# Optimization experiments

Measured on AMD Instinct MI355X. Metric: run time of the kernel, lower is better.

Reference implementation:

```python
import jax, jax.numpy as jnp
import numpy as np

T, B, INPUT, HIDDEN, OUTPUT = 512, 128, 256, 512, 128

def setup_inputs() -> dict:
    key = jax.random.key(0)
    k1, k2, k3 = jax.random.split(key, 3)
    fan_in = INPUT + HIDDEN
    bound = 1.0 / np.sqrt(fan_in)
    x = jax.random.normal(k1, (T, B, INPUT), dtype=jnp.float32)
    W = jax.random.uniform(k2, (HIDDEN, fan_in), minval=-bound, maxval=bound, dtype=jnp.float32)
    b = jax.random.uniform(k3, (HIDDEN,), minval=-bound, maxval=bound, dtype=jnp.float32)
    return {"x": x, "W": W, "b": b}

def reference(x, W, b):
    # W: [H, INPUT+H] (torch Linear layout); split into input and hidden parts
    Wx = W[:, :INPUT]   # [H, I]
    Wh = W[:, INPUT:]   # [H, H]
    h0 = jnp.zeros((x.shape[1], Wh.shape[0]), dtype=x.dtype)
    # precompute input projections for all steps: [T, B, H]
    xp = jnp.einsum('tbi,hi->tbh', x, Wx) + b

    def step(h, xp_t):
        h_new = jnp.tanh(xp_t + h @ Wh.T)
        return h_new, h_new

    _, Hs = jax.lax.scan(step, h0, xp)
    return jnp.concatenate([h0[None], Hs], axis=0)  # [T+1, B, H]
```

## Files before the change

### kernel.cpp

```cpp
#include <hip/hip_runtime.h>
#include <hip/hip_bf16.h>
#include <hip/hip_fp16.h>
#include <stdint.h>

#define T_STEPS 512
#define BATCH   128
#define NIN     256
#define HID     512

typedef _Float16 f16x2 __attribute__((ext_vector_type(2)));
typedef unsigned int u32x4 __attribute__((ext_vector_type(4)));

__device__ __forceinline__ float fdot2u(uint32_t a, uint32_t b, float c) {
#if __has_builtin(__builtin_amdgcn_fdot2)
  return __builtin_amdgcn_fdot2(__builtin_bit_cast(f16x2, a),
                                __builtin_bit_cast(f16x2, b), c, false);
#else
  __half2 ha = __builtin_bit_cast(__half2, a);
  __half2 hb = __builtin_bit_cast(__half2, b);
  return c + __half2float(ha.x) * __half2float(hb.x)
           + __half2float(ha.y) * __half2float(hb.y);
#endif
}

__device__ __forceinline__ float dot8v(u32x4 w, u32x4 x, float a) {
  a = fdot2u(w.x, x.x, a);
  a = fdot2u(w.y, x.y, a);
  a = fdot2u(w.z, x.z, a);
  a = fdot2u(w.w, x.w, a);
  return a;
}

__device__ __forceinline__ float dot8(uint4 w, uint4 x, float a) {
  a = fdot2u(w.x, x.x, a);
  a = fdot2u(w.y, x.y, a);
  a = fdot2u(w.z, x.z, a);
  a = fdot2u(w.w, x.w, a);
  return a;
}

__global__ void prep_w(const float* __restrict__ W,
                       __half* __restrict__ Wx, __half* __restrict__ Wh) {
  int idx = blockIdx.x * 256 + threadIdx.x;
  int h = idx / (NIN + HID);
  int c = idx - h * (NIN + HID);
  float v = W[idx];
  if (c < NIN) Wx[h * NIN + c] = __float2half(v);
  else         Wh[h * HID + (c - NIN)] = __float2half(v);
}

__launch_bounds__(256)
__global__ void gemm_xp(const float* __restrict__ x,
                        const __half* __restrict__ Wx,
                        const float* __restrict__ bias,
                        float* __restrict__ xp) {
  __shared__ __align__(16) __half xs[32][256];

  const int bid = blockIdx.x;
  const int m0 = (bid >> 1) * 32;
  const int n0 = (bid & 1) * 256;
  const int tid = threadIdx.x;

  {
    int r = tid >> 3, cb = (tid & 7) * 32;
    const float* src = x + (size_t)(m0 + r) * NIN + cb;
    union { __half h[8]; uint4 u; } cv;
#pragma unroll
    for (int i = 0; i < 4; ++i) {
      float4 f0 = *(const float4*)(src + i * 8);
      float4 f1 = *(const float4*)(src + i * 8 + 4);
      cv.h[0] = __float2half(f0.x); cv.h[1] = __float2half(f0.y);
      cv.h[2] = __float2half(f0.z); cv.h[3] = __float2half(f0.w);
      cv.h[4] = __float2half(f1.x); cv.h[5] = __float2half(f1.y);
      cv.h[6] = __float2half(f1.z); cv.h[7] = __float2half(f1.w);
      *(uint4*)(void*)&xs[r][cb + i * 8] = cv.u;
    }
  }
  __syncthreads();

  const int rg = tid >> 6;
  const int c0 = tid & 63;

  float acc[8][4];
#pragma unroll
  for (int r = 0; r < 8; ++r)
#pragma unroll
    for (int j = 0; j < 4; ++j) acc[r][j] = 0.f;

  for (int kc = 0; kc < NIN; kc += 32) {
    uint4 w[4][4];
#pragma unroll
    for (int j = 0; j < 4; ++j) {
      const __half* wp = Wx + (size_t)(n0 + c0 + 64 * j) * NIN + kc;
#pragma unroll
      for (int i = 0; i < 4; ++i) w[j][i] = *(const uint4*)(wp + i * 8);
    }
#pragma unroll
    for (int r = 0; r < 8; ++r) {
      uint4 xv[4];
#pragma unroll
      for (int i = 0; i < 4; ++i)
        xv[i] = *(const uint4*)(const void*)&xs[rg * 8 + r][kc + i * 8];
#pragma unroll
      for (int j = 0; j < 4; ++j)
#pragma unroll
        for (int i = 0; i < 4; ++i) acc[r][j] = dot8(w[j][i], xv[i], acc[r][j]);
    }
  }

  float bj[4];
#pragma unroll
  for (int j = 0; j < 4; ++j) bj[j] = bias[n0 + c0 + 64 * j];
#pragma unroll
  for (int r = 0; r < 8; ++r) {
    float* dst = xp + (size_t)(m0 + rg * 8 + r) * HID + n0 + c0;
#pragma unroll
    for (int j = 0; j < 4; ++j) dst[64 * j] = acc[r][j] + bj[j];
  }
}

#define HCH 72
#define PST 520
__launch_bounds__(512, 2)
__global__ void rnn_scan(const __half* __restrict__ Wh, float* io) {
  __shared__ __align__(16) char  whl[131072];
  __shared__ __align__(16) float part[8 * PST];
  __shared__ __align__(16) __half hsh[8 * HCH];

  const int b   = blockIdx.x;
  const int tid = threadIdx.x;
  const int ks  = tid & 7;
  const int rb  = tid >> 3;
  const int R0  = rb * 8;
  const __half* wbase = Wh + (size_t)R0 * HID + ks * 64;

  u32x4 wres[6][8];
#pragma unroll
  for (int r = 0; r < 6; ++r)
#pragma unroll
    for (int i = 0; i < 8; ++i)
      wres[r][i] = *(const u32x4*)(const void*)(wbase + (size_t)r * HID + i * 8);
#pragma unroll
  for (int r = 0; r < 6; ++r)
#pragma unroll
    for (int i = 0; i < 8; ++i)
      asm volatile("" : "+v"(wres[r][i]));

  const int off6 = (((rb * 2) * 8 + ks) << 7) | (ks << 4);
#pragma unroll
  for (int i = 0; i < 8; ++i) {
    u32x4 v6 = *(const u32x4*)(const void*)(wbase + (size_t)6 * HID + i * 8);
    u32x4 v7 = *(const u32x4*)(const void*)(wbase + (size_t)7 * HID + i * 8);
    *(u32x4*)(void*)(whl + (off6 ^ (i << 4)))        = v6;
    *(u32x4*)(void*)(whl + ((off6 ^ (i << 4)) + 1024)) = v7;
  }

  const int hwb = (tid >> 6) * HCH + (tid & 63);
  hsh[hwb] = __float2half(0.f);
  io[(size_t)b * HID + tid] = 0.f;
  __syncthreads();

  const u32x4* hv = (const u32x4*)(const void*)(hsh + ks * HCH);
  float* iorow = io + (size_t)BATCH * HID + (size_t)b * HID + tid;
  float* pwr = part + ks * PST + R0;

  float xpv = *iorow;

  for (int t = 0; t < T_STEPS; ++t) {
    float xpn = 0.f;
    if (t + 1 < T_STEPS) xpn = iorow[BATCH * HID];

    u32x4 hj[8];
#pragma unroll
    for (int i = 0; i < 8; ++i) hj[i] = hv[i];

    float a6 = 0.f, a7 = 0.f;
#pragma unroll
    for (int i = 0; i < 8; ++i) {
      u32x4 w6 = *(const u32x4*)(const void*)(whl + (off6 ^ (i << 4)));
      u32x4 w7 = *(const u32x4*)(const void*)(whl + ((off6 ^ (i << 4)) + 1024));
      a6 = dot8v(w6, hj[i], a6);
      a7 = dot8v(w7, hj[i], a7);
    }

    float acc[6];
#pragma unroll
    for (int r = 0; r < 6; ++r) {
      float a = 0.f;
#pragma unroll
      for (int i = 0; i < 8; ++i) a = dot8v(wres[r][i], hj[i], a);
      acc[r] = a;
    }

    {
      float4 p0 = make_float4(acc[0], acc[1], acc[2], acc[3]);
      float4 p1 = make_float4(acc[4], acc[5], a6, a7);
      *(float4*)(void*)(pwr)     = p0;
      *(float4*)(void*)(pwr + 4) = p1;
    }
    __syncthreads();

    float s = 0.f;
#pragma unroll
    for (int k = 0; k < 8; ++k) s += part[k * PST + tid];
    s += xpv;
    float e  = __expf(fminf(fmaxf(2.f * s, -40.f), 40.f));
    float hn = (e - 1.f) / (e + 1.f);
    *iorow = hn;
    hsh[hwb] = __float2half(hn);
    __syncthreads();

    xpv = xpn;
    iorow += BATCH * HID;
  }
}

extern "C" void kernel_launch(void* const* d_in, const int* in_sizes, int n_in,
                              void* d_out, int out_size, void* d_ws, size_t ws_size,
                              hipStream_t stream) {
  const float* x    = (const float*)d_in[0];
  const float* W    = (const float*)d_in[1];
  const float* bias = (const float*)d_in[2];

  char* ws = (char*)d_ws;
  __half* Wx = (__half*)ws;
  __half* Wh = (__half*)(ws + 262144);

  float* io = (float*)d_out;
  float* xp = io + (size_t)BATCH * HID;

  prep_w<<<1536, 256, 0, stream>>>(W, Wx, Wh);
  gemm_xp<<<4096, 256, 0, stream>>>(x, Wx, bias, xp);
  rnn_scan<<<BATCH, 512, 0, stream>>>(Wh, io);
}
```

Before: 1.156 ms.

## Replace shared-memory partial reduction with warp shuffles and double-buffer hidden state

```diff
diff --git a/kernel.cpp b/kernel.cpp
--- a/kernel.cpp
+++ b/kernel.cpp
@@ -120,12 +120,11 @@
 }
 
 #define HCH 72
-#define PST 520
 __launch_bounds__(512, 2)
 __global__ void rnn_scan(const __half* __restrict__ Wh, float* io) {
-  __shared__ __align__(16) char  whl[131072];
-  __shared__ __align__(16) float part[8 * PST];
-  __shared__ __align__(16) __half hsh[8 * HCH];
+  __shared__ __align__(16) char   whl[131072];
+  __shared__ __align__(16) __half hA[8 * HCH];
+  __shared__ __align__(16) __half hB[8 * HCH];
 
   const int b   = blockIdx.x;
   const int tid = threadIdx.x;
@@ -134,83 +133,89 @@
   const int R0  = rb * 8;
   const __half* wbase = Wh + (size_t)R0 * HID + ks * 64;
 
-  u32x4 wres[6][8];
+  uint32_t wres[6][32];
 #pragma unroll
   for (int r = 0; r < 6; ++r)
 #pragma unroll
-    for (int i = 0; i < 8; ++i)
-      wres[r][i] = *(const u32x4*)(const void*)(wbase + (size_t)r * HID + i * 8);
+    for (int i = 0; i < 8; ++i) {
+      u32x4 q = *(const u32x4*)(const void*)(wbase + (size_t)r * HID + i * 8);
+      wres[r][4 * i + 0] = q.x; wres[r][4 * i + 1] = q.y;
+      wres[r][4 * i + 2] = q.z; wres[r][4 * i + 3] = q.w;
+    }
 #pragma unroll
   for (int r = 0; r < 6; ++r)
 #pragma unroll
-    for (int i = 0; i < 8; ++i)
-      asm volatile("" : "+v"(wres[r][i]));
+    for (int j = 0; j < 32; ++j)
+      asm volatile("" : "+v"(wres[r][j]));
 
   const int off6 = (((rb * 2) * 8 + ks) << 7) | (ks << 4);
 #pragma unroll
   for (int i = 0; i < 8; ++i) {
     u32x4 v6 = *(const u32x4*)(const void*)(wbase + (size_t)6 * HID + i * 8);
     u32x4 v7 = *(const u32x4*)(const void*)(wbase + (size_t)7 * HID + i * 8);
-    *(u32x4*)(void*)(whl + (off6 ^ (i << 4)))        = v6;
+    *(u32x4*)(void*)(whl + (off6 ^ (i << 4)))          = v6;
     *(u32x4*)(void*)(whl + ((off6 ^ (i << 4)) + 1024)) = v7;
   }
 
   const int hwb = (tid >> 6) * HCH + (tid & 63);
-  hsh[hwb] = __float2half(0.f);
+  hA[hwb] = __float2half(0.f);
   io[(size_t)b * HID + tid] = 0.f;
   __syncthreads();
 
-  const u32x4* hv = (const u32x4*)(const void*)(hsh + ks * HCH);
   float* iorow = io + (size_t)BATCH * HID + (size_t)b * HID + tid;
-  float* pwr = part + ks * PST + R0;
-
   float xpv = *iorow;
 
-  for (int t = 0; t < T_STEPS; ++t) {
+  auto do_step = [&](const __half* rd, __half* wr, float xpi, float* iop,
+                     int t) -> float {
     float xpn = 0.f;
-    if (t + 1 < T_STEPS) xpn = iorow[BATCH * HID];
-
-    u32x4 hj[8];
-#pragma unroll
-    for (int i = 0; i < 8; ++i) hj[i] = hv[i];
-
-    float a6 = 0.f, a7 = 0.f;
+    if (t + 1 < T_STEPS) xpn = iop[BATCH * HID];
+
+    float acc[8];
+#pragma unroll
+    for (int r = 0; r < 8; ++r) acc[r] = 0.f;
+
 #pragma unroll
     for (int i = 0; i < 8; ++i) {
+      u32x4 hj = *(const u32x4*)(const void*)((const char*)rd + ks * 144 + i * 16);
       u32x4 w6 = *(const u32x4*)(const void*)(whl + (off6 ^ (i << 4)));
       u32x4 w7 = *(const u32x4*)(const void*)(whl + ((off6 ^ (i << 4)) + 1024));
-      a6 = dot8v(w6, hj[i], a6);
-      a7 = dot8v(w7, hj[i], a7);
-    }
-
-    float acc[6];
-#pragma unroll
-    for (int r = 0; r < 6; ++r) {
-      float a = 0.f;
-#pragma unroll
-      for (int i = 0; i < 8; ++i) a = dot8v(wres[r][i], hj[i], a);
-      acc[r] = a;
-    }
-
-    {
-      float4 p0 = make_float4(acc[0], acc[1], acc[2], acc[3]);
-      float4 p1 = make_float4(acc[4], acc[5], a6, a7);
-      *(float4*)(void*)(pwr)     = p0;
-      *(float4*)(void*)(pwr + 4) = p1;
-    }
-    __syncthreads();
-
-    float s = 0.f;
-#pragma unroll
-    for (int k = 0; k < 8; ++k) s += part[k * PST + tid];
-    s += xpv;
+#pragma unroll
+      for (int r = 0; r < 6; ++r) {
+        acc[r] = fdot2u(wres[r][4 * i + 0], hj.x, acc[r]);
+        acc[r] = fdot2u(wres[r][4 * i + 1], hj.y, acc[r]);
+        acc[r] = fdot2u(wres[r][4 * i + 2], hj.z, acc[r]);
+        acc[r] = fdot2u(wres[r][4 * i + 3], hj.w, acc[r]);
+      }
+      acc[6] = dot8v(w6, hj, acc[6]);
+      acc[7] = dot8v(w7, hj, acc[7]);
+    }
+
+    float sum[8];
+#pragma unroll
+    for (int r = 0; r < 8; ++r) {
+      float v = acc[r];
+      v += __shfl_xor(v, 1);
+      v += __shfl_xor(v, 2);
+      v += __shfl_xor(v, 4);
+      sum[r] = v;
+    }
+    float s = sum[0];
+#pragma unroll
+    for (int r = 1; r < 8; ++r) s = (ks == r) ? sum[r] : s;
+
+    s += xpi;
     float e  = __expf(fminf(fmaxf(2.f * s, -40.f), 40.f));
     float hn = (e - 1.f) / (e + 1.f);
-    *iorow = hn;
-    hsh[hwb] = __float2half(hn);
+    *iop = hn;
+    wr[hwb] = __float2half(hn);
     __syncthreads();
-
-    xpv = xpn;
+    return xpn;
+  };
+
+  for (int t = 0; t < T_STEPS; t += 2) {
+    xpv = do_step(hA, hB, xpv, iorow, t);
+    iorow += BATCH * HID;
+    xpv = do_step(hB, hA, xpv, iorow, t + 1);
     iorow += BATCH * HID;
   }
 }
```

After: 1.234 ms. 1.07x slower.
